# Optimization experiments

Hardware: AMD Instinct MI355X
Metric: run time of the kernel (lower is better)

Reference implementation:

```python
import jax, jax.numpy as jnp
import numpy as np

N, M, D = 4096, 8192, 512

def setup_inputs() -> dict:
    key = jax.random.key(0)
    k1, k2, k3, k4 = jax.random.split(key, 4)
    X = jax.random.normal(k1, (N, D), dtype=jnp.float32)
    SV = jax.random.normal(k2, (M, D), dtype=jnp.float32)
    DC = jax.random.normal(k3, (1, M), dtype=jnp.float32)
    IC = jax.random.normal(k4, (1,), dtype=jnp.float32)
    gamma = jnp.float32(1.0 / D)
    return {"X": X, "SV": SV, "DC": DC, "IC": IC, "gamma": gamma}

def reference(X, SV, DC, IC, gamma):
    # Squared pairwise L2 distances via GEMM expansion (same math as
    # ||SV - x||^2 without materializing the [N, M, D] broadcast tensor):
    # d2[n, m] = ||x_n||^2 + ||sv_m||^2 - 2 * x_n . sv_m
    x2 = jnp.sum(X * X, axis=1)          # [N]
    sv2 = jnp.sum(SV * SV, axis=1)       # [M]
    cross = jnp.einsum("nd,md->nm", X, SV)  # [N, M]
    d2 = jnp.maximum(x2[:, None] + sv2[None, :] - 2.0 * cross, 0.0)
    k = jnp.exp(-gamma * d2)             # RBF kernel values [N, M]
    # Weighted reduction over support vectors + intercept -> decision values [N]
    return jnp.sum(k * DC, axis=1) + IC
```

## Files before the change

### kernel.cpp

```cpp
#include <hip/hip_runtime.h>
#include <stdint.h>

#define NN 4096
#define MM 8192
#define DD 512
#define NKT 16

typedef __bf16 bf16x8 __attribute__((ext_vector_type(8)));
typedef __bf16 bf16x4 __attribute__((ext_vector_type(4)));
typedef float f32x4 __attribute__((ext_vector_type(4)));
typedef float f32x16 __attribute__((ext_vector_type(16)));

__device__ __forceinline__ void load_lds16(const void* g, void* l) {
  __builtin_amdgcn_global_load_lds(
      (const __attribute__((address_space(1))) unsigned int*)g,
      (__attribute__((address_space(3))) unsigned int*)l, 16, 0, 0);
}

template <int CTRL>
__device__ __forceinline__ float dpp_radd(float x) {
  int xi = __float_as_int(x);
  int mv = __builtin_amdgcn_update_dpp(xi, xi, CTRL, 0xF, 0xF, false);
  return x + __int_as_float(mv);
}
__device__ __forceinline__ float swz_add_xor16(float x) {
  int sv = __builtin_amdgcn_ds_swizzle(__float_as_int(x), 0x401F);
  return x + __int_as_float(sv);
}

__global__ __launch_bounds__(256) void convert_norm_kernel(
    const float* __restrict__ X, const float* __restrict__ SV,
    __bf16* __restrict__ Xb, __bf16* __restrict__ SVb,
    float* __restrict__ x2, float* __restrict__ sv2,
    float* __restrict__ out, const float* __restrict__ IC) {
  int wid = blockIdx.x * 4 + (threadIdx.x >> 6);
  int lane = threadIdx.x & 63;
  const float* src;
  __bf16* dst;
  float* nrm;
  if (wid < NN) {
    src = X + (size_t)wid * DD;
    dst = Xb + (size_t)wid * DD;
    nrm = x2 + wid;
    if (lane == 0) out[wid] = IC[0];
  } else {
    int r = wid - NN;
    src = SV + (size_t)r * DD;
    dst = SVb + (size_t)r * DD;
    nrm = sv2 + r;
  }
  const f32x4* s = (const f32x4*)src;
  f32x4 a = s[lane];
  f32x4 b = s[lane + 64];
  float sum = a.x * a.x + a.y * a.y + a.z * a.z + a.w * a.w +
              b.x * b.x + b.y * b.y + b.z * b.z + b.w * b.w;
  bf16x4 ca = {(__bf16)a.x, (__bf16)a.y, (__bf16)a.z, (__bf16)a.w};
  bf16x4 cb = {(__bf16)b.x, (__bf16)b.y, (__bf16)b.z, (__bf16)b.w};
  *(bf16x4*)(dst + 4 * lane) = ca;
  *(bf16x4*)(dst + 256 + 4 * lane) = cb;
#pragma unroll
  for (int m = 32; m >= 1; m >>= 1) sum += __shfl_xor(sum, m, 64);
  if (lane == 0) *nrm = sum;
}

__device__ __forceinline__ void stage_tile(const bf16x8* __restrict__ srcA,
                                           const bf16x8* __restrict__ srcB,
                                           bf16x8* AsD, bf16x8* BsD, int tid,
                                           int tt) {
  const bf16x8* sa = srcA + tt * 4;
  const bf16x8* sb = srcB + tt * 4;
  load_lds16(sa, AsD + tid);
  load_lds16(sa + 8192, AsD + 512 + tid);
  load_lds16(sb, BsD + tid);
  load_lds16(sb + 8192, BsD + 512 + tid);
}

__device__ __forceinline__ void compute_tile(f32x16 (&acc)[4][2],
                                             const bf16x8* AsB,
                                             const bf16x8* BsB, int aoff,
                                             int boff, int lhi, int rsw) {
#pragma unroll
  for (int ks = 0; ks < 2; ++ks) {
    const int gs = (2 * ks + lhi) ^ rsw;
    bf16x8 a0 = AsB[aoff + gs];
    bf16x8 a1 = AsB[aoff + 128 + gs];
    bf16x8 a2 = AsB[aoff + 256 + gs];
    bf16x8 a3 = AsB[aoff + 384 + gs];
    bf16x8 b0 = BsB[boff + gs];
    bf16x8 b1 = BsB[boff + 128 + gs];
    __builtin_amdgcn_s_setprio(1);
    acc[0][0] = __builtin_amdgcn_mfma_f32_32x32x16_bf16(a0, b0, acc[0][0], 0, 0, 0);
    acc[0][1] = __builtin_amdgcn_mfma_f32_32x32x16_bf16(a0, b1, acc[0][1], 0, 0, 0);
    acc[1][0] = __builtin_amdgcn_mfma_f32_32x32x16_bf16(a1, b0, acc[1][0], 0, 0, 0);
    acc[1][1] = __builtin_amdgcn_mfma_f32_32x32x16_bf16(a1, b1, acc[1][1], 0, 0, 0);
    acc[2][0] = __builtin_amdgcn_mfma_f32_32x32x16_bf16(a2, b0, acc[2][0], 0, 0, 0);
    acc[2][1] = __builtin_amdgcn_mfma_f32_32x32x16_bf16(a2, b1, acc[2][1], 0, 0, 0);
    acc[3][0] = __builtin_amdgcn_mfma_f32_32x32x16_bf16(a3, b0, acc[3][0], 0, 0, 0);
    acc[3][1] = __builtin_amdgcn_mfma_f32_32x32x16_bf16(a3, b1, acc[3][1], 0, 0, 0);
    __builtin_amdgcn_s_setprio(0);
  }
}

__global__ __launch_bounds__(512, 2) void rbf_gemm_kernel(
    const bf16x8* __restrict__ Xb, const bf16x8* __restrict__ SVb,
    const float* __restrict__ x2, const float* __restrict__ sv2,
    const float* __restrict__ DC, const float* __restrict__ gamma_p,
    float* __restrict__ out) {
  __shared__ bf16x8 As[4096];
  __shared__ bf16x8 Bs[4096];

  const int t = threadIdx.x;
  const int lane = t & 63;
  const int wave = t >> 6;
  const int l31 = lane & 31;
  const int lhi = lane >> 5;
  const int wave_n = wave & 1;
  const int wave_m = wave >> 1;
  const int n0 = blockIdx.x * 256;
  const int m0 = blockIdx.y * 256;

  const int rsw = (l31 >> 1) & 3;
  const int aoff = (wave_n * 128 + l31) * 4;
  const int boff = (wave_m * 64 + l31) * 4;

  const int row0 = t >> 2;
  const int gsw = (t & 3) ^ ((row0 >> 1) & 3);
  const bf16x8* srcA = Xb + (size_t)(n0 + row0) * 64 + gsw;
  const bf16x8* srcB = SVb + (size_t)(m0 + row0) * 64 + gsw;

  f32x16 acc[4][2];
#pragma unroll
  for (int i = 0; i < 4; ++i)
#pragma unroll
    for (int j = 0; j < 2; ++j)
#pragma unroll
      for (int r = 0; r < 16; ++r) acc[i][j][r] = 0.0f;

  stage_tile(srcA, srcB, As, Bs, t, 0);
  stage_tile(srcA, srcB, As + 1024, Bs + 1024, t, 1);
  stage_tile(srcA, srcB, As + 2048, Bs + 2048, t, 2);
  __syncthreads();

#pragma unroll 4
  for (int kt = 0; kt < 12; ++kt) {
    const int bn = (kt + 3) & 3;
    stage_tile(srcA, srcB, As + bn * 1024, Bs + bn * 1024, t, kt + 3);
    const int bc = kt & 3;
    compute_tile(acc, As + bc * 1024, Bs + bc * 1024, aoff, boff, lhi, rsw);
    asm volatile("s_waitcnt vmcnt(8)" ::: "memory");
    __builtin_amdgcn_s_barrier();
  }
  stage_tile(srcA, srcB, As + 3072, Bs + 3072, t, 15);
  compute_tile(acc, As, Bs, aoff, boff, lhi, rsw);
  asm volatile("s_waitcnt vmcnt(8)" ::: "memory");
  __builtin_amdgcn_s_barrier();
  compute_tile(acc, As + 1024, Bs + 1024, aoff, boff, lhi, rsw);
  asm volatile("s_waitcnt vmcnt(4)" ::: "memory");
  __builtin_amdgcn_s_barrier();
  compute_tile(acc, As + 2048, Bs + 2048, aoff, boff, lhi, rsw);
  asm volatile("s_waitcnt vmcnt(0)" ::: "memory");
  __builtin_amdgcn_s_barrier();
  compute_tile(acc, As + 3072, Bs + 3072, aoff, boff, lhi, rsw);

  const float g = gamma_p[0];
  const float c2 = g * 1.4426950408889634f;

  float sv2v[2], dcv[2];
  const int colb = m0 + wave_m * 64 + l31;
  sv2v[0] = sv2[colb];
  dcv[0] = DC[colb];
  sv2v[1] = sv2[colb + 32];
  dcv[1] = DC[colb + 32];

#pragma unroll
  for (int i = 0; i < 4; ++i) {
    const int rowb = n0 + wave_n * 128 + i * 32 + 4 * lhi;
    float val[16];
#pragma unroll
    for (int g4 = 0; g4 < 4; ++g4) {
      f32x4 xv = *(const f32x4*)(x2 + rowb + 8 * g4);
#pragma unroll
      for (int r2 = 0; r2 < 4; ++r2) {
        const int reg = g4 * 4 + r2;
        float v = 0.0f;
#pragma unroll
        for (int j = 0; j < 2; ++j) {
          float d2 = xv[r2] + sv2v[j] - 2.0f * acc[i][j][reg];
          d2 = fmaxf(d2, 0.0f);
          v += exp2f(-c2 * d2) * dcv[j];
        }
        val[reg] = v;
      }
    }
#pragma unroll
    for (int reg = 0; reg < 16; ++reg) {
      float v = val[reg];
      v = dpp_radd<0x121>(v);
      v = dpp_radd<0x122>(v);
      v = dpp_radd<0x124>(v);
      v = dpp_radd<0x128>(v);
      val[reg] = swz_add_xor16(v);
    }
    if (l31 == 0) {
#pragma unroll
      for (int g4 = 0; g4 < 4; ++g4)
#pragma unroll
        for (int r2 = 0; r2 < 4; ++r2)
          atomicAdd(&out[rowb + 8 * g4 + r2], val[g4 * 4 + r2]);
    }
  }
}

extern "C" void kernel_launch(void* const* d_in, const int* in_sizes, int n_in,
                              void* d_out, int out_size, void* d_ws, size_t ws_size,
                              hipStream_t stream) {
  const float* X = (const float*)d_in[0];
  const float* SV = (const float*)d_in[1];
  const float* DC = (const float*)d_in[2];
  const float* IC = (const float*)d_in[3];
  const float* gamma = (const float*)d_in[4];
  float* out = (float*)d_out;

  char* ws = (char*)d_ws;
  __bf16* Xb = (__bf16*)ws;
  __bf16* SVb = (__bf16*)(ws + (size_t)NN * DD * 2);
  float* x2 = (float*)(ws + (size_t)(NN + MM) * DD * 2);
  float* sv2 = x2 + NN;

  convert_norm_kernel<<<(NN + MM) / 4, 256, 0, stream>>>(X, SV, Xb, SVb, x2, sv2, out, IC);
  dim3 grid(NN / 256, MM / 256);
  rbf_gemm_kernel<<<grid, 512, 0, stream>>>((const bf16x8*)Xb, (const bf16x8*)SVb,
                                            x2, sv2, DC, gamma, out);
}
```

Before: 150.5 us.

## Split each k-tile into two barrier-separated phases interleaving loads with MFMAs

Each 32-wide k-tile's compute is split into two half-k phases. Each phase issues its LDS fragment reads, then half of the next tile's global-to-LDS loads (A in the first phase, B in the second). It then hits a barrier, waits on LDS, and runs the MFMA block under raised priority, with a sched_barrier to pin the order. The prologue now waits only for the first tile instead of a full sync, and the loop covers 13 iterations with a shorter tail. The aim is to spread memory issue across the MFMA stream and keep waves in lock-step, at the cost of twice as many barriers per tile.

New measurement: 152.0 us. About the same (+1.0%).

```diff
diff --git a/kernel.cpp b/kernel.cpp
--- a/kernel.cpp
+++ b/kernel.cpp
@@ -4,7 +4,6 @@
 #define NN 4096
 #define MM 8192
 #define DD 512
-#define NKT 16
 
 typedef __bf16 bf16x8 __attribute__((ext_vector_type(8)));
 typedef __bf16 bf16x4 __attribute__((ext_vector_type(4)));
@@ -63,42 +62,38 @@
   if (lane == 0) *nrm = sum;
 }
 
-__device__ __forceinline__ void stage_tile(const bf16x8* __restrict__ srcA,
-                                           const bf16x8* __restrict__ srcB,
-                                           bf16x8* AsD, bf16x8* BsD, int tid,
-                                           int tt) {
-  const bf16x8* sa = srcA + tt * 4;
-  const bf16x8* sb = srcB + tt * 4;
-  load_lds16(sa, AsD + tid);
-  load_lds16(sa + 8192, AsD + 512 + tid);
-  load_lds16(sb, BsD + tid);
-  load_lds16(sb + 8192, BsD + 512 + tid);
-}
-
-__device__ __forceinline__ void compute_tile(f32x16 (&acc)[4][2],
-                                             const bf16x8* AsB,
-                                             const bf16x8* BsB, int aoff,
-                                             int boff, int lhi, int rsw) {
-#pragma unroll
-  for (int ks = 0; ks < 2; ++ks) {
-    const int gs = (2 * ks + lhi) ^ rsw;
-    bf16x8 a0 = AsB[aoff + gs];
-    bf16x8 a1 = AsB[aoff + 128 + gs];
-    bf16x8 a2 = AsB[aoff + 256 + gs];
-    bf16x8 a3 = AsB[aoff + 384 + gs];
-    bf16x8 b0 = BsB[boff + gs];
-    bf16x8 b1 = BsB[boff + 128 + gs];
-    __builtin_amdgcn_s_setprio(1);
-    acc[0][0] = __builtin_amdgcn_mfma_f32_32x32x16_bf16(a0, b0, acc[0][0], 0, 0, 0);
-    acc[0][1] = __builtin_amdgcn_mfma_f32_32x32x16_bf16(a0, b1, acc[0][1], 0, 0, 0);
-    acc[1][0] = __builtin_amdgcn_mfma_f32_32x32x16_bf16(a1, b0, acc[1][0], 0, 0, 0);
-    acc[1][1] = __builtin_amdgcn_mfma_f32_32x32x16_bf16(a1, b1, acc[1][1], 0, 0, 0);
-    acc[2][0] = __builtin_amdgcn_mfma_f32_32x32x16_bf16(a2, b0, acc[2][0], 0, 0, 0);
-    acc[2][1] = __builtin_amdgcn_mfma_f32_32x32x16_bf16(a2, b1, acc[2][1], 0, 0, 0);
-    acc[3][0] = __builtin_amdgcn_mfma_f32_32x32x16_bf16(a3, b0, acc[3][0], 0, 0, 0);
-    acc[3][1] = __builtin_amdgcn_mfma_f32_32x32x16_bf16(a3, b1, acc[3][1], 0, 0, 0);
-    __builtin_amdgcn_s_setprio(0);
-  }
+template <bool STAGE, int VM, bool ENDBAR>
+__device__ __forceinline__ void run_phase(
+    f32x16 (&acc)[4][2], const bf16x8* __restrict__ Ab,
+    const bf16x8* __restrict__ Bb, int aoff, int boff, int gs,
+    const bf16x8* sg0, bf16x8* sl0, const bf16x8* sg1, bf16x8* sl1) {
+  bf16x8 a0 = Ab[aoff + gs];
+  bf16x8 a1 = Ab[aoff + 128 + gs];
+  bf16x8 a2 = Ab[aoff + 256 + gs];
+  bf16x8 a3 = Ab[aoff + 384 + gs];
+  bf16x8 b0 = Bb[boff + gs];
+  bf16x8 b1 = Bb[boff + 128 + gs];
+  if (STAGE) {
+    load_lds16(sg0, sl0);
+    load_lds16(sg1, sl1);
+  }
+  __builtin_amdgcn_s_barrier();
+  asm volatile("s_waitcnt lgkmcnt(0)" ::: "memory");
+  __builtin_amdgcn_sched_barrier(0);
+  __builtin_amdgcn_s_setprio(1);
+  acc[0][0] = __builtin_amdgcn_mfma_f32_32x32x16_bf16(a0, b0, acc[0][0], 0, 0, 0);
+  acc[0][1] = __builtin_amdgcn_mfma_f32_32x32x16_bf16(a0, b1, acc[0][1], 0, 0, 0);
+  acc[1][0] = __builtin_amdgcn_mfma_f32_32x32x16_bf16(a1, b0, acc[1][0], 0, 0, 0);
+  acc[1][1] = __builtin_amdgcn_mfma_f32_32x32x16_bf16(a1, b1, acc[1][1], 0, 0, 0);
+  acc[2][0] = __builtin_amdgcn_mfma_f32_32x32x16_bf16(a2, b0, acc[2][0], 0, 0, 0);
+  acc[2][1] = __builtin_amdgcn_mfma_f32_32x32x16_bf16(a2, b1, acc[2][1], 0, 0, 0);
+  acc[3][0] = __builtin_amdgcn_mfma_f32_32x32x16_bf16(a3, b0, acc[3][0], 0, 0, 0);
+  acc[3][1] = __builtin_amdgcn_mfma_f32_32x32x16_bf16(a3, b1, acc[3][1], 0, 0, 0);
+  __builtin_amdgcn_s_setprio(0);
+  if (VM == 8) asm volatile("s_waitcnt vmcnt(8)" ::: "memory");
+  if (VM == 4) asm volatile("s_waitcnt vmcnt(4)" ::: "memory");
+  if (VM == 0) asm volatile("s_waitcnt vmcnt(0)" ::: "memory");
+  if (ENDBAR) __builtin_amdgcn_s_barrier();
 }
 
 __global__ __launch_bounds__(512, 2) void rbf_gemm_kernel(
@@ -122,6 +117,8 @@
   const int rsw = (l31 >> 1) & 3;
   const int aoff = (wave_n * 128 + l31) * 4;
   const int boff = (wave_m * 64 + l31) * 4;
+  const int g0 = lhi ^ rsw;
+  const int g1 = (2 + lhi) ^ rsw;
 
   const int row0 = t >> 2;
   const int gsw = (t & 3) ^ ((row0 >> 1) & 3);
@@ -136,31 +133,43 @@
 #pragma unroll
       for (int r = 0; r < 16; ++r) acc[i][j][r] = 0.0f;
 
-  stage_tile(srcA, srcB, As, Bs, t, 0);
-  stage_tile(srcA, srcB, As + 1024, Bs + 1024, t, 1);
-  stage_tile(srcA, srcB, As + 2048, Bs + 2048, t, 2);
-  __syncthreads();
-
-#pragma unroll 4
-  for (int kt = 0; kt < 12; ++kt) {
-    const int bn = (kt + 3) & 3;
-    stage_tile(srcA, srcB, As + bn * 1024, Bs + bn * 1024, t, kt + 3);
-    const int bc = kt & 3;
-    compute_tile(acc, As + bc * 1024, Bs + bc * 1024, aoff, boff, lhi, rsw);
-    asm volatile("s_waitcnt vmcnt(8)" ::: "memory");
-    __builtin_amdgcn_s_barrier();
-  }
-  stage_tile(srcA, srcB, As + 3072, Bs + 3072, t, 15);
-  compute_tile(acc, As, Bs, aoff, boff, lhi, rsw);
+#pragma unroll
+  for (int tt = 0; tt < 3; ++tt) {
+    load_lds16(srcA + tt * 4, As + tt * 1024 + t);
+    load_lds16(srcA + tt * 4 + 8192, As + tt * 1024 + 512 + t);
+    load_lds16(srcB + tt * 4, Bs + tt * 1024 + t);
+    load_lds16(srcB + tt * 4 + 8192, Bs + tt * 1024 + 512 + t);
+  }
   asm volatile("s_waitcnt vmcnt(8)" ::: "memory");
   __builtin_amdgcn_s_barrier();
-  compute_tile(acc, As + 1024, Bs + 1024, aoff, boff, lhi, rsw);
-  asm volatile("s_waitcnt vmcnt(4)" ::: "memory");
-  __builtin_amdgcn_s_barrier();
-  compute_tile(acc, As + 2048, Bs + 2048, aoff, boff, lhi, rsw);
-  asm volatile("s_waitcnt vmcnt(0)" ::: "memory");
-  __builtin_amdgcn_s_barrier();
-  compute_tile(acc, As + 3072, Bs + 3072, aoff, boff, lhi, rsw);
+
+#pragma unroll 4
+  for (int kt = 0; kt < 13; ++kt) {
+    const int bc = kt & 3;
+    const int bn = (kt + 3) & 3;
+    const bf16x8* Ab = As + bc * 1024;
+    const bf16x8* Bb = Bs + bc * 1024;
+    const bf16x8* sa = srcA + (kt + 3) * 4;
+    const bf16x8* sb = srcB + (kt + 3) * 4;
+    run_phase<true, -1, true>(acc, Ab, Bb, aoff, boff, g0, sa,
+                              As + bn * 1024 + t, sa + 8192,
+                              As + bn * 1024 + 512 + t);
+    run_phase<true, 8, true>(acc, Ab, Bb, aoff, boff, g1, sb,
+                             Bs + bn * 1024 + t, sb + 8192,
+                             Bs + bn * 1024 + 512 + t);
+  }
+  run_phase<false, -1, true>(acc, As + 1024, Bs + 1024, aoff, boff, g0,
+                             nullptr, nullptr, nullptr, nullptr);
+  run_phase<false, 4, true>(acc, As + 1024, Bs + 1024, aoff, boff, g1,
+                            nullptr, nullptr, nullptr, nullptr);
+  run_phase<false, -1, true>(acc, As + 2048, Bs + 2048, aoff, boff, g0,
+                             nullptr, nullptr, nullptr, nullptr);
+  run_phase<false, 0, true>(acc, As + 2048, Bs + 2048, aoff, boff, g1,
+                            nullptr, nullptr, nullptr, nullptr);
+  run_phase<false, -1, true>(acc, As + 3072, Bs + 3072, aoff, boff, g0,
+                             nullptr, nullptr, nullptr, nullptr);
+  run_phase<false, -1, false>(acc, As + 3072, Bs + 3072, aoff, boff, g1,
+                              nullptr, nullptr, nullptr, nullptr);
 
   const float g = gamma_p[0];
   const float c2 = g * 1.4426950408889634f;
```
